# Kernel optimization log

Hardware: AMD Instinct MI355X
Metric: run time of the kernel (lower is better)

## Reference

```python
import jax, jax.numpy as jnp
import numpy as np

N_NODES = 100000
IN_CH = 256
OUT_CH = 128
HEADS = 1
N_EDGES = 1600000
NEG_SLOPE = 0.2
EPS = 1e-16


def setup_inputs() -> dict:
    key = jax.random.key(0)
    ks = jax.random.split(key, 6)
    x = jax.random.normal(ks[0], (N_NODES, IN_CH), dtype=jnp.float32)
    edge_index = jax.random.randint(ks[1], (2, N_EDGES), 0, N_NODES, dtype=jnp.int64)
    # xavier-ish scaled params
    lin_src = jax.random.normal(ks[2], (IN_CH, OUT_CH), dtype=jnp.float32) * (1.414 * (2.0 / (IN_CH + OUT_CH)) ** 0.5)
    att_src = jax.random.normal(ks[3], (1, HEADS, OUT_CH), dtype=jnp.float32) * 0.1
    att_dst = jax.random.normal(ks[4], (1, HEADS, OUT_CH), dtype=jnp.float32) * 0.1
    bias = jnp.zeros((HEADS * OUT_CH,), dtype=jnp.float32)
    return {"x": x, "edge_index": edge_index, "lin_src": lin_src,
            "att_src": att_src, "att_dst": att_dst, "bias": bias}


def reference(x, edge_index, lin_src, att_src, att_dst, bias):
    N = x.shape[0]
    # shared projection (lin_dst is lin_src when in_channels is an int)
    xp = (x @ lin_src).reshape(N, HEADS, OUT_CH)  # [N, H, C]

    # add_self_loops: drop existing self-edges (via mask) and append N loop edges
    src, dst = edge_index[0], edge_index[1]
    loop = jnp.arange(N, dtype=edge_index.dtype)
    src_all = jnp.concatenate([src, loop])
    dst_all = jnp.concatenate([dst, loop])
    valid = jnp.concatenate([src != dst, jnp.ones((N,), dtype=bool)])  # [E+N]

    # per-node attention logits
    alpha_src = jnp.sum(xp * att_src, axis=-1)  # [N, H]
    alpha_dst = jnp.sum(xp * att_dst, axis=-1)  # [N, H]
    alpha = alpha_src[src_all] + alpha_dst[dst_all]  # [E+N, H]
    alpha = jax.nn.leaky_relu(alpha, NEG_SLOPE)

    # scatter softmax over incoming edges of each dst node (global-max stabilized,
    # matching the original src.max() over all retained edges)
    amax = jnp.max(jnp.where(valid[:, None], alpha, -jnp.inf))
    ex = jnp.exp(alpha - amax) * valid[:, None].astype(alpha.dtype)
    denom = jax.ops.segment_sum(ex, dst_all, num_segments=N)  # [N, H]
    alpha = ex / (denom[dst_all] + EPS)  # [E+N, H]

    # weighted aggregation
    weighted = xp[src_all] * alpha[..., None]  # [E+N, H, C]
    out = jax.ops.segment_sum(weighted, dst_all, num_segments=N)  # [N, H, C]

    out = out.reshape(N, HEADS * OUT_CH) + bias  # concat=True
    return out
```

## Files before the change

kernel.cpp:

```cpp
#include <hip/hip_runtime.h>
#include <cstdint>
#include <cstddef>

#define IN_CH 256
#define OUT_CH 128
#define NEG_SLOPE 0.2f
#define EPS 1e-16f

#define NXCD 8
#define XCC_ID_HWREG 6164

typedef __attribute__((ext_vector_type(8))) short bf16x8;
typedef __attribute__((ext_vector_type(4))) float f32x4;

__device__ __forceinline__ unsigned short f2bf(float f) {
    unsigned int u = __float_as_uint(f);
    return (unsigned short)((u + 0x7fffu + ((u >> 16) & 1u)) >> 16);
}

__global__ __launch_bounds__(256) void convert_w_kernel(const float* __restrict__ w,
                                                        unsigned short* __restrict__ wt)
{
    const int n = blockIdx.x;
    const int k = threadIdx.x;
    wt[(size_t)n * IN_CH + k] = f2bf(w[(size_t)k * OUT_CH + n]);
}

__device__ __forceinline__ void gemm_body(
    int bid, const float* __restrict__ x, const unsigned short* __restrict__ wt,
    const float* __restrict__ att_s, const float* __restrict__ att_d,
    unsigned short* __restrict__ xpb, float* __restrict__ asrc, float* __restrict__ adst,
    int M)
{
    const int tid  = threadIdx.x;
    const int wv   = tid >> 6;
    const int lane = tid & 63;
    const int lm   = lane & 15;
    const int quad = lane >> 4;
    const int arow = bid * 64 + wv * 16 + lm;
    const bool av  = arow < M;
    const float* xrow = x + (size_t)arow * IN_CH + quad * 8;

    f32x4 acc[8];
#pragma unroll
    for (int t = 0; t < 8; ++t) acc[t] = (f32x4){0.f, 0.f, 0.f, 0.f};

#pragma unroll
    for (int kk = 0; kk < 8; ++kk) {
        const int k0 = kk * 32;
        bf16x8 af = {0, 0, 0, 0, 0, 0, 0, 0};
        if (av) {
            float4 a0 = *(const float4*)(xrow + k0);
            float4 a1 = *(const float4*)(xrow + k0 + 4);
            af[0] = (short)f2bf(a0.x); af[1] = (short)f2bf(a0.y);
            af[2] = (short)f2bf(a0.z); af[3] = (short)f2bf(a0.w);
            af[4] = (short)f2bf(a1.x); af[5] = (short)f2bf(a1.y);
            af[6] = (short)f2bf(a1.z); af[7] = (short)f2bf(a1.w);
        }
#pragma unroll
        for (int t = 0; t < 8; ++t) {
            bf16x8 bf = *(const bf16x8*)(wt + (size_t)(16 * t + lm) * IN_CH + k0 + quad * 8);
            acc[t] = __builtin_amdgcn_mfma_f32_16x16x32_bf16(af, bf, acc[t], 0, 0, 0);
        }
    }

    float asw[8], adw[8];
#pragma unroll
    for (int t = 0; t < 8; ++t) {
        asw[t] = att_s[16 * t + lm];
        adw[t] = att_d[16 * t + lm];
    }
#pragma unroll
    for (int r = 0; r < 4; ++r) {
        const int orow = bid * 64 + wv * 16 + quad * 4 + r;
        if (orow < M) {
            float ps = 0.f, pd = 0.f;
            unsigned short* xr = xpb + (size_t)orow * OUT_CH + lm;
#pragma unroll
            for (int t = 0; t < 8; ++t) {
                float v = acc[t][r];
                xr[16 * t] = f2bf(v);
                ps += v * asw[t];
                pd += v * adw[t];
            }
#pragma unroll
            for (int m = 1; m < 16; m <<= 1) {
                ps += __shfl_xor(ps, m, 16);
                pd += __shfl_xor(pd, m, 16);
            }
            if (lm == 0) { asrc[orow] = ps; adst[orow] = pd; }
        }
    }
}

__device__ __forceinline__ void hist_body(
    int bid, int nblk,
    const int* __restrict__ src, const int* __restrict__ dst,
    int* __restrict__ deg_part, int N, int* __restrict__ pw, int E)
{
    const int xcd = (int)(__builtin_amdgcn_s_getreg(XCC_ID_HWREG) & 7u);
    int* mydeg = deg_part + (size_t)xcd * N;
    const int T = nblk * 256;
    const int e0 = bid * 256 + threadIdx.x;
#pragma unroll
    for (int k = 0; k < 2; ++k) {
        const int e = e0 + k * T;
        if (e < E) {
            int s = src[e], d = dst[e];
            if (s != d) {
                int pos = __hip_atomic_fetch_add(&mydeg[d], 1,
                                                 __ATOMIC_RELAXED,
                                                 __HIP_MEMORY_SCOPE_WORKGROUP);
                pw[e] = (xcd << 27) | pos;
            }
        }
    }
}

__global__ __launch_bounds__(256) void fused_gemm_hist_kernel(
    const float* __restrict__ x, const unsigned short* __restrict__ wt,
    const float* __restrict__ att_s, const float* __restrict__ att_d,
    unsigned short* __restrict__ xpb, float* __restrict__ asrc, float* __restrict__ adst,
    int M,
    const int* __restrict__ src, const int* __restrict__ dst,
    int* __restrict__ deg_part, int* __restrict__ pw, int E,
    int hist_blocks)
{
    if ((int)blockIdx.x < hist_blocks)
        hist_body(blockIdx.x, hist_blocks, src, dst, deg_part, M, pw, E);
    else
        gemm_body(blockIdx.x - hist_blocks, x, wt, att_s, att_d, xpb, asrc, adst, M);
}

#define SCAN_NB 256
#define SCAN_NT 256

__global__ __launch_bounds__(SCAN_NT) void scan_partial_kernel(
    const int* __restrict__ deg_part, int* __restrict__ bsum, int N)
{
    __shared__ int sh[SCAN_NT];
    const int chunk = (N + SCAN_NB - 1) / SCAN_NB;
    const int sub   = (chunk + SCAN_NT - 1) / SCAN_NT;
    const int b0 = blockIdx.x * chunk;
    const int t0 = b0 + threadIdx.x * sub;
    const int t1 = min(min(b0 + chunk, t0 + sub), N);
    int s = 0;
    for (int i = t0; i < t1; ++i) {
#pragma unroll
        for (int xx = 0; xx < NXCD; ++xx) s += deg_part[(size_t)xx * N + i];
    }
    sh[threadIdx.x] = s;
    __syncthreads();
    for (int off = SCAN_NT / 2; off > 0; off >>= 1) {
        if (threadIdx.x < off) sh[threadIdx.x] += sh[threadIdx.x + off];
        __syncthreads();
    }
    if (threadIdx.x == 0) bsum[blockIdx.x] = sh[0];
}

__global__ __launch_bounds__(SCAN_NB) void scan_blocksums_kernel(
    const int* __restrict__ bsum, int* __restrict__ boff,
    int* __restrict__ row_ptr, int N)
{
    __shared__ int sh[SCAN_NB];
    const int t = threadIdx.x;
    sh[t] = bsum[t];
    __syncthreads();
    for (int off = 1; off < SCAN_NB; off <<= 1) {
        int v = (t >= off) ? sh[t - off] : 0;
        __syncthreads();
        sh[t] += v;
        __syncthreads();
    }
    boff[t] = (t == 0) ? 0 : sh[t - 1];
    if (t == SCAN_NB - 1) row_ptr[N] = sh[t];
}

__global__ __launch_bounds__(SCAN_NT) void scan_fill_kernel(
    int* __restrict__ deg_part, const int* __restrict__ boff,
    int* __restrict__ row_ptr, int N)
{
    __shared__ int sh[SCAN_NT];
    const int chunk = (N + SCAN_NB - 1) / SCAN_NB;
    const int sub   = (chunk + SCAN_NT - 1) / SCAN_NT;
    const int b0 = blockIdx.x * chunk;
    const int t0 = b0 + threadIdx.x * sub;
    const int t1 = min(min(b0 + chunk, t0 + sub), N);
    int s = 0;
    for (int i = t0; i < t1; ++i) {
#pragma unroll
        for (int xx = 0; xx < NXCD; ++xx) s += deg_part[(size_t)xx * N + i];
    }
    sh[threadIdx.x] = s;
    __syncthreads();
    for (int off = 1; off < SCAN_NT; off <<= 1) {
        int v = (threadIdx.x >= off) ? sh[threadIdx.x - off] : 0;
        __syncthreads();
        sh[threadIdx.x] += v;
        __syncthreads();
    }
    int run = boff[blockIdx.x] + ((threadIdx.x == 0) ? 0 : sh[threadIdx.x - 1]);
    for (int i = t0; i < t1; ++i) {
        row_ptr[i] = run;
#pragma unroll
        for (int xx = 0; xx < NXCD; ++xx) {
            int c = deg_part[(size_t)xx * N + i];
            deg_part[(size_t)xx * N + i] = run;
            run += c;
        }
    }
}

__global__ __launch_bounds__(256) void scatter_kernel(
    const int* __restrict__ src, const int* __restrict__ dst,
    const int* __restrict__ deg_part, int N, const int* __restrict__ pw,
    int* __restrict__ col, int E, int nblk)
{
    const int T = nblk * 256;
    const int e0 = blockIdx.x * 256 + threadIdx.x;
#pragma unroll
    for (int k = 0; k < 8; ++k) {
        const int e = e0 + k * T;
        if (e < E) {
            int s = src[e], d = dst[e];
            if (s != d) {
                unsigned int p = (unsigned int)pw[e];
                int xcd = (int)(p >> 27);
                int pos = (int)(p & 0x07ffffffu);
                col[deg_part[(size_t)xcd * N + d] + pos] = s;
            }
        }
    }
}

__global__ __launch_bounds__(256) void aggregate_kernel(
    const unsigned short* __restrict__ xpb, const float* __restrict__ asrc,
    const float* __restrict__ adst, const int* __restrict__ row_ptr,
    const int* __restrict__ col, const float* __restrict__ bias,
    float* __restrict__ out, int N)
{
    const int n = (int)((blockIdx.x * blockDim.x + threadIdx.x) >> 6);
    const int lane = threadIdx.x & 63;
    if (n >= N) return;
    const float a_d = adst[n];
    const unsigned int* xpw = (const unsigned int*)xpb;

    float ax0 = 0.f, ay0 = 0.f, ax1 = 0.f, ay1 = 0.f;
    float ax2 = 0.f, ay2 = 0.f, ax3 = 0.f, ay3 = 0.f;
    float den = 0.f;

    {
        float lg = asrc[n] + a_d;
        lg = (lg > 0.f) ? lg : lg * NEG_SLOPE;
        float ex = __expf(lg);
        den += ex;
        unsigned int v = xpw[(size_t)n * 64 + lane];
        ax0 += ex * __uint_as_float(v << 16);
        ay0 += ex * __uint_as_float(v & 0xffff0000u);
    }

    const int beg = row_ptr[n], end = row_ptr[n + 1];
    for (int base = beg; base < end; base += 64) {
        const int idx = base + lane;
        int s = 0; float ex = 0.f;
        if (idx < end) {
            s = col[idx];
            float lg = asrc[s] + a_d;
            lg = (lg > 0.f) ? lg : lg * NEG_SLOPE;
            ex = __expf(lg);
        }
        const int cnt = min(64, end - base);
        int j = 0;
        for (; j + 4 <= cnt; j += 4) {
            float e0 = __shfl(ex, j, 64),     e1 = __shfl(ex, j + 1, 64);
            float e2 = __shfl(ex, j + 2, 64), e3 = __shfl(ex, j + 3, 64);
            int   s0 = __shfl(s, j, 64),      s1 = __shfl(s, j + 1, 64);
            int   s2 = __shfl(s, j + 2, 64),  s3 = __shfl(s, j + 3, 64);
            unsigned int v0 = xpw[(size_t)s0 * 64 + lane];
            unsigned int v1 = xpw[(size_t)s1 * 64 + lane];
            unsigned int v2 = xpw[(size_t)s2 * 64 + lane];
            unsigned int v3 = xpw[(size_t)s3 * 64 + lane];
            den += (e0 + e1) + (e2 + e3);
            ax0 += e0 * __uint_as_float(v0 << 16);
            ay0 += e0 * __uint_as_float(v0 & 0xffff0000u);
            ax1 += e1 * __uint_as_float(v1 << 16);
            ay1 += e1 * __uint_as_float(v1 & 0xffff0000u);
            ax2 += e2 * __uint_as_float(v2 << 16);
            ay2 += e2 * __uint_as_float(v2 & 0xffff0000u);
            ax3 += e3 * __uint_as_float(v3 << 16);
            ay3 += e3 * __uint_as_float(v3 & 0xffff0000u);
        }
        for (; j < cnt; ++j) {
            float e0 = __shfl(ex, j, 64);
            int   s0 = __shfl(s, j, 64);
            unsigned int v0 = xpw[(size_t)s0 * 64 + lane];
            den += e0;
            ax0 += e0 * __uint_as_float(v0 << 16);
            ay0 += e0 * __uint_as_float(v0 & 0xffff0000u);
        }
    }

    const float inv = 1.f / (den + EPS);
    const float2 bv = ((const float2*)bias)[lane];
    float2 o;
    o.x = ((ax0 + ax1) + (ax2 + ax3)) * inv + bv.x;
    o.y = ((ay0 + ay1) + (ay2 + ay3)) * inv + bv.y;
    ((float2*)out)[(size_t)n * 64 + lane] = o;
}

extern "C" void kernel_launch(void* const* d_in, const int* in_sizes, int n_in,
                              void* d_out, int out_size, void* d_ws, size_t ws_size,
                              hipStream_t stream)
{
    const float* x     = (const float*)d_in[0];
    const int*   ei    = (const int*)d_in[1];
    const float* w     = (const float*)d_in[2];
    const float* att_s = (const float*)d_in[3];
    const float* att_d = (const float*)d_in[4];
    const float* bias  = (const float*)d_in[5];
    float* out = (float*)d_out;

    const int N = in_sizes[0] / IN_CH;
    const int E = in_sizes[1] / 2;
    const int* src = ei;
    const int* dst = ei + E;

    char* p = (char*)d_ws;
    auto take = [&](size_t bytes) { char* q = p; p += (bytes + 255) & ~size_t(255); return q; };
    unsigned short* xpb = (unsigned short*)take((size_t)N * OUT_CH * 2);
    unsigned short* wt  = (unsigned short*)take((size_t)OUT_CH * IN_CH * 2);
    float* asrc   = (float*)take((size_t)N * 4);
    float* adst   = (float*)take((size_t)N * 4);
    int*   deg_part = (int*)take((size_t)NXCD * N * 4);
    int*   row_ptr  = (int*)take((size_t)(N + 1) * 4);
    int*   bsum   = (int*)take(SCAN_NB * 4);
    int*   boff   = (int*)take(SCAN_NB * 4);
    int*   pw     = (int*)take((size_t)E * 4);
    int*   col    = (int*)take((size_t)E * 4);

    hipMemsetAsync(deg_part, 0, (size_t)NXCD * N * 4, stream);
    convert_w_kernel<<<OUT_CH, IN_CH, 0, stream>>>(w, wt);

    const int gemm_blocks = (N + 63) / 64;
    const int hist_blocks = (E + 256 * 2 - 1) / (256 * 2);
    fused_gemm_hist_kernel<<<hist_blocks + gemm_blocks, 256, 0, stream>>>(
        x, wt, att_s, att_d, xpb, asrc, adst, N,
        src, dst, deg_part, pw, E, hist_blocks);

    scan_partial_kernel<<<SCAN_NB, SCAN_NT, 0, stream>>>(deg_part, bsum, N);
    scan_blocksums_kernel<<<1, SCAN_NB, 0, stream>>>(bsum, boff, row_ptr, N);
    scan_fill_kernel<<<SCAN_NB, SCAN_NT, 0, stream>>>(deg_part, boff, row_ptr, N);

    const int sc_blocks = (E + 256 * 8 - 1) / (256 * 8);
    scatter_kernel<<<sc_blocks, 256, 0, stream>>>(src, dst, deg_part, N, pw, col, E, sc_blocks);

    aggregate_kernel<<<(N + 3) / 4, 256, 0, stream>>>(
        xpb, asrc, adst, row_ptr, col, bias, out, N);
}
```

Measured before the change: 383.3 us.

## Split fused GEMM/histogram, pre-convert x to bf16, precompute edge exps in scatter

Splits the fused GEMM+histogram kernel into separate launches and adds a pass that converts x to bf16 before the GEMM, so the GEMM reads bf16 directly. The scatter kernel now computes each edge's leaky-relu exp and stores it next to col, so the aggregate kernel no longer gathers asrc per edge or evaluates exp. In exchange the change adds an extra full pass over x (read fp32, write bf16), a new E-sized float array that is written and then read, and loses the overlap between histogram and GEMM blocks.

```diff
diff --git a/kernel.cpp b/kernel.cpp
--- a/kernel.cpp
+++ b/kernel.cpp
@@ -26,12 +26,26 @@
     wt[(size_t)n * IN_CH + k] = f2bf(w[(size_t)k * OUT_CH + n]);
 }
 
-__device__ __forceinline__ void gemm_body(
-    int bid, const float* __restrict__ x, const unsigned short* __restrict__ wt,
+__global__ __launch_bounds__(256) void convert_x_kernel(
+    const float* __restrict__ x, unsigned short* __restrict__ xb, long long nquad)
+{
+    const long long stride = (long long)gridDim.x * blockDim.x;
+    for (long long i = (long long)blockIdx.x * blockDim.x + threadIdx.x;
+         i < nquad; i += stride) {
+        float4 v = ((const float4*)x)[i];
+        ushort4 o;
+        o.x = f2bf(v.x); o.y = f2bf(v.y); o.z = f2bf(v.z); o.w = f2bf(v.w);
+        ((ushort4*)xb)[i] = o;
+    }
+}
+
+__global__ __launch_bounds__(256) void gemm_kernel(
+    const unsigned short* __restrict__ xb, const unsigned short* __restrict__ wt,
     const float* __restrict__ att_s, const float* __restrict__ att_d,
     unsigned short* __restrict__ xpb, float* __restrict__ asrc, float* __restrict__ adst,
     int M)
 {
+    const int bid  = blockIdx.x;
     const int tid  = threadIdx.x;
     const int wv   = tid >> 6;
     const int lane = tid & 63;
@@ -39,7 +53,7 @@
     const int quad = lane >> 4;
     const int arow = bid * 64 + wv * 16 + lm;
     const bool av  = arow < M;
-    const float* xrow = x + (size_t)arow * IN_CH + quad * 8;
+    const unsigned short* xrow = xb + (size_t)arow * IN_CH + quad * 8;
 
     f32x4 acc[8];
 #pragma unroll
@@ -49,14 +63,7 @@
     for (int kk = 0; kk < 8; ++kk) {
         const int k0 = kk * 32;
         bf16x8 af = {0, 0, 0, 0, 0, 0, 0, 0};
-        if (av) {
-            float4 a0 = *(const float4*)(xrow + k0);
-            float4 a1 = *(const float4*)(xrow + k0 + 4);
-            af[0] = (short)f2bf(a0.x); af[1] = (short)f2bf(a0.y);
-            af[2] = (short)f2bf(a0.z); af[3] = (short)f2bf(a0.w);
-            af[4] = (short)f2bf(a1.x); af[5] = (short)f2bf(a1.y);
-            af[6] = (short)f2bf(a1.z); af[7] = (short)f2bf(a1.w);
-        }
+        if (av) af = *(const bf16x8*)(xrow + k0);
 #pragma unroll
         for (int t = 0; t < 8; ++t) {
             bf16x8 bf = *(const bf16x8*)(wt + (size_t)(16 * t + lm) * IN_CH + k0 + quad * 8);
@@ -93,17 +100,16 @@
     }
 }
 
-__device__ __forceinline__ void hist_body(
-    int bid, int nblk,
+__global__ __launch_bounds__(256) void hist_kernel(
     const int* __restrict__ src, const int* __restrict__ dst,
-    int* __restrict__ deg_part, int N, int* __restrict__ pw, int E)
+    int* __restrict__ deg_part, int N, int* __restrict__ pw, int E, int nblk)
 {
     const int xcd = (int)(__builtin_amdgcn_s_getreg(XCC_ID_HWREG) & 7u);
     int* mydeg = deg_part + (size_t)xcd * N;
     const int T = nblk * 256;
-    const int e0 = bid * 256 + threadIdx.x;
-#pragma unroll
-    for (int k = 0; k < 2; ++k) {
+    const int e0 = blockIdx.x * 256 + threadIdx.x;
+#pragma unroll
+    for (int k = 0; k < 4; ++k) {
         const int e = e0 + k * T;
         if (e < E) {
             int s = src[e], d = dst[e];
@@ -117,21 +123,6 @@
     }
 }
 
-__global__ __launch_bounds__(256) void fused_gemm_hist_kernel(
-    const float* __restrict__ x, const unsigned short* __restrict__ wt,
-    const float* __restrict__ att_s, const float* __restrict__ att_d,
-    unsigned short* __restrict__ xpb, float* __restrict__ asrc, float* __restrict__ adst,
-    int M,
-    const int* __restrict__ src, const int* __restrict__ dst,
-    int* __restrict__ deg_part, int* __restrict__ pw, int E,
-    int hist_blocks)
-{
-    if ((int)blockIdx.x < hist_blocks)
-        hist_body(blockIdx.x, hist_blocks, src, dst, deg_part, M, pw, E);
-    else
-        gemm_body(blockIdx.x - hist_blocks, x, wt, att_s, att_d, xpb, asrc, adst, M);
-}
-
 #define SCAN_NB 256
 #define SCAN_NT 256
 
@@ -214,7 +205,8 @@
 __global__ __launch_bounds__(256) void scatter_kernel(
     const int* __restrict__ src, const int* __restrict__ dst,
     const int* __restrict__ deg_part, int N, const int* __restrict__ pw,
-    int* __restrict__ col, int E, int nblk)
+    const float* __restrict__ asrc, const float* __restrict__ adst,
+    int* __restrict__ col, float* __restrict__ exa, int E, int nblk)
 {
     const int T = nblk * 256;
     const int e0 = blockIdx.x * 256 + threadIdx.x;
@@ -227,7 +219,11 @@
                 unsigned int p = (unsigned int)pw[e];
                 int xcd = (int)(p >> 27);
                 int pos = (int)(p & 0x07ffffffu);
-                col[deg_part[(size_t)xcd * N + d] + pos] = s;
+                int slot = deg_part[(size_t)xcd * N + d] + pos;
+                float lg = asrc[s] + adst[d];
+                lg = (lg > 0.f) ? lg : lg * NEG_SLOPE;
+                col[slot] = s;
+                exa[slot] = __expf(lg);
             }
         }
     }
@@ -236,13 +232,12 @@
 __global__ __launch_bounds__(256) void aggregate_kernel(
     const unsigned short* __restrict__ xpb, const float* __restrict__ asrc,
     const float* __restrict__ adst, const int* __restrict__ row_ptr,
-    const int* __restrict__ col, const float* __restrict__ bias,
-    float* __restrict__ out, int N)
+    const int* __restrict__ col, const float* __restrict__ exa,
+    const float* __restrict__ bias, float* __restrict__ out, int N)
 {
     const int n = (int)((blockIdx.x * blockDim.x + threadIdx.x) >> 6);
     const int lane = threadIdx.x & 63;
     if (n >= N) return;
-    const float a_d = adst[n];
     const unsigned int* xpw = (const unsigned int*)xpb;
 
     float ax0 = 0.f, ay0 = 0.f, ax1 = 0.f, ay1 = 0.f;
@@ -250,7 +245,7 @@
     float den = 0.f;
 
     {
-        float lg = asrc[n] + a_d;
+        float lg = asrc[n] + adst[n];
         lg = (lg > 0.f) ? lg : lg * NEG_SLOPE;
         float ex = __expf(lg);
         den += ex;
@@ -264,10 +259,8 @@
         const int idx = base + lane;
         int s = 0; float ex = 0.f;
         if (idx < end) {
-            s = col[idx];
-            float lg = asrc[s] + a_d;
-            lg = (lg > 0.f) ? lg : lg * NEG_SLOPE;
-            ex = __expf(lg);
+            s  = col[idx];
+            ex = exa[idx];
         }
         const int cnt = min(64, end - base);
         int j = 0;
@@ -329,6 +322,7 @@
     auto take = [&](size_t bytes) { char* q = p; p += (bytes + 255) & ~size_t(255); return q; };
     unsigned short* xpb = (unsigned short*)take((size_t)N * OUT_CH * 2);
     unsigned short* wt  = (unsigned short*)take((size_t)OUT_CH * IN_CH * 2);
+    unsigned short* xb  = (unsigned short*)take((size_t)N * IN_CH * 2);
     float* asrc   = (float*)take((size_t)N * 4);
     float* adst   = (float*)take((size_t)N * 4);
     int*   deg_part = (int*)take((size_t)NXCD * N * 4);
@@ -337,23 +331,28 @@
     int*   boff   = (int*)take(SCAN_NB * 4);
     int*   pw     = (int*)take((size_t)E * 4);
     int*   col    = (int*)take((size_t)E * 4);
+    float* exa    = (float*)take((size_t)E * 4);
 
     hipMemsetAsync(deg_part, 0, (size_t)NXCD * N * 4, stream);
     convert_w_kernel<<<OUT_CH, IN_CH, 0, stream>>>(w, wt);
 
+    const long long nquad = (long long)N * IN_CH / 4;
+    convert_x_kernel<<<2048, 256, 0, stream>>>(x, xb, nquad);
+
+    const int hist_blocks = (E + 256 * 4 - 1) / (256 * 4);
+    hist_kernel<<<hist_blocks, 256, 0, stream>>>(src, dst, deg_part, N, pw, E, hist_blocks);
+
     const int gemm_blocks = (N + 63) / 64;
-    const int hist_blocks = (E + 256 * 2 - 1) / (256 * 2);
-    fused_gemm_hist_kernel<<<hist_blocks + gemm_blocks, 256, 0, stream>>>(
-        x, wt, att_s, att_d, xpb, asrc, adst, N,
-        src, dst, deg_part, pw, E, hist_blocks);
+    gemm_kernel<<<gemm_blocks, 256, 0, stream>>>(xb, wt, att_s, att_d, xpb, asrc, adst, N);
 
     scan_partial_kernel<<<SCAN_NB, SCAN_NT, 0, stream>>>(deg_part, bsum, N);
     scan_blocksums_kernel<<<1, SCAN_NB, 0, stream>>>(bsum, boff, row_ptr, N);
     scan_fill_kernel<<<SCAN_NB, SCAN_NT, 0, stream>>>(deg_part, boff, row_ptr, N);
 
     const int sc_blocks = (E + 256 * 8 - 1) / (256 * 8);
-    scatter_kernel<<<sc_blocks, 256, 0, stream>>>(src, dst, deg_part, N, pw, col, E, sc_blocks);
+    scatter_kernel<<<sc_blocks, 256, 0, stream>>>(src, dst, deg_part, N, pw,
+                                                  asrc, adst, col, exa, E, sc_blocks);
 
     aggregate_kernel<<<(N + 3) / 4, 256, 0, stream>>>(
-        xpb, asrc, adst, row_ptr, col, bias, out, N);
-}
+        xpb, asrc, adst, row_ptr, col, exa, bias, out, N);
+}
```

Result: slower. 446.4 us (+16.5%).
